# Kernel optimization log

Measured on AMD Instinct MI355X. Metric: run time of the kernel, lower is better.

The kernel has to match this reference:

```python
import jax, jax.numpy as jnp
import numpy as np

N_NODES = 50000
N_EDGES = 800000
H = 128            # node_hidden_size
T = 2              # num_prop_rounds


def setup_inputs() -> dict:
    key = jax.random.key(0)
    ks = jax.random.split(key, 10)
    hv = jax.random.normal(ks[0], (N_NODES, H), dtype=jnp.float32)
    he = jax.random.normal(ks[1], (N_EDGES, 1), dtype=jnp.float32)
    src = jax.random.randint(ks[2], (N_EDGES,), 0, N_NODES, dtype=jnp.int32)
    dst = jax.random.randint(ks[3], (N_EDGES,), 0, N_NODES, dtype=jnp.int32)
    # per-round params, stacked on leading T axis; small scale to avoid gate saturation
    W_msg = jax.random.normal(ks[4], (T, 2 * H, 2 * H + 1), dtype=jnp.float32) * 0.05
    b_msg = jax.random.normal(ks[5], (T, 2 * H), dtype=jnp.float32) * 0.05
    W_ih = jax.random.normal(ks[6], (T, 3 * H, 2 * H), dtype=jnp.float32) * 0.05
    W_hh = jax.random.normal(ks[7], (T, 3 * H, H), dtype=jnp.float32) * 0.05
    b_ih = jax.random.normal(ks[8], (T, 3 * H), dtype=jnp.float32) * 0.05
    b_hh = jax.random.normal(ks[9], (T, 3 * H), dtype=jnp.float32) * 0.05
    return dict(hv=hv, he=he, src=src, dst=dst, W_msg=W_msg, b_msg=b_msg,
                W_ih=W_ih, W_hh=W_hh, b_ih=b_ih, b_hh=b_hh)


def _gru_cell(x, h, W_ih, W_hh, b_ih, b_hh):
    # torch.nn.GRUCell math
    gi = x @ W_ih.T + b_ih          # [N, 3H]
    gh = h @ W_hh.T + b_hh          # [N, 3H]
    i_r, i_z, i_n = jnp.split(gi, 3, axis=1)
    h_r, h_z, h_n = jnp.split(gh, 3, axis=1)
    r = jax.nn.sigmoid(i_r + h_r)
    z = jax.nn.sigmoid(i_z + h_z)
    n = jnp.tanh(i_n + r * h_n)
    return (1.0 - z) * n + z * h


def reference(hv, he, src, dst, W_msg, b_msg, W_ih, W_hh, b_ih, b_hh):
    n_nodes = hv.shape[0]
    for t in range(T):
        # per-edge message input: concat([hv_dst, hv_src, he])  [E, 2H+1]
        msg_in = jnp.concatenate([hv[dst], hv[src], he], axis=1)
        edge_act = msg_in @ W_msg[t].T + b_msg[t]          # [E, 2H]
        # ragged sum-reduce over incoming edges (deg-0 nodes get zeros)
        a = jax.ops.segment_sum(edge_act, dst, num_segments=n_nodes)  # [N, 2H]
        hv = _gru_cell(a, hv, W_ih[t], W_hh[t], b_ih[t], b_hh[t])
    return hv
```

## Files before the change

### kernel.cpp

```cpp
#include <hip/hip_runtime.h>
#include <cstdint>
#include <cstddef>

#define N_NODES 50000
#define N_EDGES 800000
#define HDIM 128
#define TROUNDS 2
#define NTILES 3125
#define PACK_PER_T (416 * 64)
#define PACK_BLOCKS ((TROUNDS * PACK_PER_T) / 256)
#define CAST_BLOCKS ((N_NODES * HDIM / 4 + 255) / 256)
#define MAXDEG 64
#define NBUK 196
#define BCAP 4608
#define BCE 2048
#define NBC ((N_EDGES + BCE - 1) / BCE)

typedef __attribute__((ext_vector_type(8))) _Float16 half8v;
typedef __attribute__((ext_vector_type(2))) _Float16 half2v;
typedef __attribute__((ext_vector_type(4))) float f32x4;
typedef unsigned short ushort_t;
typedef unsigned long long u64;

#define GLD_LDS(gp, lp)                                                        \
  __builtin_amdgcn_global_load_lds(                                            \
      (__attribute__((address_space(1))) const void*)(gp),                     \
      (__attribute__((address_space(3))) void*)(lp), 16, 0, 0)

static __device__ __forceinline__ float sigmoidf_(float x) {
  return 1.0f / (1.0f + __expf(-x));
}
static __device__ __forceinline__ float tanhf_(float x) {
  float xc = fminf(15.0f, fmaxf(-15.0f, x));
  float a = __expf(2.0f * xc);
  return (a - 1.0f) / (a + 1.0f);
}
static __device__ __forceinline__ float f16bits2f(uint32_t hb) {
  ushort_t u = (ushort_t)hb;
  _Float16 h;
  __builtin_memcpy(&h, &u, 2);
  return (float)h;
}

__global__ void pack_cast(const float* __restrict__ Wmsg, const float* __restrict__ Wih,
                          const float* __restrict__ Whh, const float* __restrict__ hv,
                          _Float16* __restrict__ W1p, _Float16* __restrict__ W2p,
                          float* __restrict__ we, _Float16* __restrict__ hvh,
                          int* __restrict__ bcur) {
  if (blockIdx.x == 0 && threadIdx.x < NBUK) bcur[threadIdx.x] = 0;
  if (blockIdx.x >= PACK_BLOCKS) {
    int i = (blockIdx.x - PACK_BLOCKS) * 256 + threadIdx.x;
    if (i >= N_NODES * HDIM / 4) return;
    float4 v = reinterpret_cast<const float4*>(hv)[i];
    half2v o0, o1;
    o0[0] = (_Float16)v.x; o0[1] = (_Float16)v.y;
    o1[0] = (_Float16)v.z; o1[1] = (_Float16)v.w;
    reinterpret_cast<half2v*>(hvh)[i * 2] = o0;
    reinterpret_cast<half2v*>(hvh)[i * 2 + 1] = o1;
    return;
  }
  int g = blockIdx.x * 256 + threadIdx.x;
  if (g < TROUNDS * 256) {
    int t = g >> 8, j = g & 255;
    we[g] = Wmsg[((size_t)t * 256 + j) * 257 + 256];
  }
  int t = g / PACK_PER_T;
  int r = g % PACK_PER_T;
  int lane = r & 63;
  int fr = r >> 6;
  const float* srcp;
  _Float16* dstp;
  if (fr < 128) {
    int jt = fr >> 3, kt = fr & 7;
    int j = jt * 16 + (lane & 15);
    int k = kt * 32 + ((lane >> 4) << 3);
    srcp = Wmsg + (size_t)t * 256 * 257 + (size_t)j * 257 + k;
    dstp = W1p + ((size_t)t * 128 + fr) * 512 + lane * 8;
  } else {
    int fr2 = fr - 128;
    int chunk = fr2 / 12, idx = fr2 % 12;
    int jt = chunk / 3, pp = chunk % 3;
    int j = pp * 128 + jt * 16 + (lane & 15);
    int k;
    if (idx < 8) {
      k = idx * 32 + ((lane >> 4) << 3);
      srcp = Wih + (size_t)t * 384 * 256 + (size_t)j * 256 + k;
    } else {
      k = (idx - 8) * 32 + ((lane >> 4) << 3);
      srcp = Whh + (size_t)t * 384 * 128 + (size_t)j * 128 + k;
    }
    dstp = W2p + ((size_t)t * 288 + fr2) * 512 + lane * 8;
  }
  #pragma unroll
  for (int e = 0; e < 8; ++e) dstp[e] = (_Float16)srcp[e];
}

__global__ __launch_bounds__(256) void bin_count(
    const int* __restrict__ src, const int* __restrict__ dst,
    const float* __restrict__ he, int* __restrict__ bcur, u64* __restrict__ barr) {
  __shared__ int hist[256];
  __shared__ int incl[256];
  __shared__ int cur[256];
  __shared__ int gbase[256];
  __shared__ u64 staged[BCE];
  const int tid = threadIdx.x;
  const int e0 = blockIdx.x * BCE;
  const int tot = min(BCE, N_EDGES - e0);

  hist[tid] = 0;
  __syncthreads();

  u64 rec[BCE / 256];
  int nmine = 0;
  #pragma unroll
  for (int q = 0; q < BCE / 256; ++q) {
    int e = e0 + q * 256 + tid;
    if (e < N_EDGES) {
      uint32_t d = (uint32_t)dst[e];
      uint32_t s = (uint32_t)src[e];
      _Float16 hh = (_Float16)he[e];
      ushort_t hb;
      __builtin_memcpy(&hb, &hh, 2);
      rec[nmine] = ((u64)d << 32) | ((u64)hb << 16) | (u64)s;
      atomicAdd(&hist[d >> 8], 1);
      ++nmine;
    }
  }
  __syncthreads();

  incl[tid] = hist[tid];
  __syncthreads();
  for (int off = 1; off < 256; off <<= 1) {
    int v = incl[tid];
    int a = (tid >= off) ? incl[tid - off] : 0;
    __syncthreads();
    incl[tid] = v + a;
    __syncthreads();
  }
  cur[tid] = incl[tid] - hist[tid];
  __syncthreads();

  for (int q = 0; q < nmine; ++q) {
    int b = (int)(rec[q] >> 40);
    int pos = atomicAdd(&cur[b], 1);
    staged[pos] = rec[q];
  }
  if (tid < NBUK && hist[tid] > 0) gbase[tid] = atomicAdd(&bcur[tid], hist[tid]);
  __syncthreads();

  for (int i = tid; i < tot; i += 256) {
    u64 r = staged[i];
    int b = (int)(r >> 40);
    int excl = incl[b] - hist[b];
    barr[(size_t)b * BCAP + gbase[b] + (i - excl)] = r;
  }
}

__global__ __launch_bounds__(256) void bin_place(
    const int* __restrict__ bcur, const u64* __restrict__ barr,
    uint32_t* __restrict__ csr, int* __restrict__ deg_i) {
  __shared__ int lcnt[256];
  const int b = blockIdx.x;
  const int tid = threadIdx.x;
  const int cnt = bcur[b];
  lcnt[tid] = 0;
  __syncthreads();
  const u64* bp = barr + (size_t)b * BCAP;
  for (int i = tid; i < cnt; i += 256) {
    u64 r = bp[i];
    int d = (int)((r >> 32) & 0xffffu);
    int slot = atomicAdd(&lcnt[d & 255], 1);
    if (slot < MAXDEG) csr[(size_t)d * MAXDEG + slot] = (uint32_t)r;
  }
  __syncthreads();
  int node = b * 256 + tid;
  if (node < N_NODES) deg_i[node] = min(lcnt[tid], MAXDEG);
}

__global__ void gather_h(const _Float16* __restrict__ hvh, const int* __restrict__ deg_i,
                         const uint32_t* __restrict__ csr, _Float16* __restrict__ S_h,
                         float* __restrict__ hsum, float* __restrict__ deg_f, int n) {
  int wid = (int)((blockIdx.x * blockDim.x + threadIdx.x) >> 6);
  int lane = threadIdx.x & 63;
  if (wid >= n) return;
  int deg = deg_i[wid];
  uint32_t ent = (lane < deg) ? csr[(size_t)wid * MAXDEG + lane] : 0u;
  float a0 = 0.f, a1 = 0.f, hs = 0.f;
  int k = 0;
  for (; k + 7 < deg; k += 8) {
    uint32_t ee[8];
    #pragma unroll
    for (int q = 0; q < 8; ++q) ee[q] = __shfl(ent, k + q);
    half2v vv[8];
    #pragma unroll
    for (int q = 0; q < 8; ++q)
      vv[q] = *reinterpret_cast<const half2v*>(hvh + (size_t)(ee[q] & 0xffffu) * HDIM + lane * 2);
    #pragma unroll
    for (int q = 0; q < 8; ++q) {
      a0 += (float)vv[q][0];
      a1 += (float)vv[q][1];
      hs += f16bits2f(ee[q] >> 16);
    }
  }
  for (; k < deg; ++k) {
    uint32_t e0 = __shfl(ent, k);
    half2v v0 = *reinterpret_cast<const half2v*>(hvh + (size_t)(e0 & 0xffffu) * HDIM + lane * 2);
    a0 += (float)v0[0];
    a1 += (float)v0[1];
    hs += f16bits2f(e0 >> 16);
  }
  half2v o;
  o[0] = (_Float16)a0;
  o[1] = (_Float16)a1;
  *reinterpret_cast<half2v*>(S_h + (size_t)wid * HDIM + lane * 2) = o;
  if (lane == 0) hsum[wid] = hs;
  if (lane == 1) deg_f[wid] = (float)deg;
}

__global__ __launch_bounds__(256, 4) void u1_kernel(
    const _Float16* __restrict__ hvh, const _Float16* __restrict__ S_h,
    const float* __restrict__ deg_f, const float* __restrict__ hsum,
    const _Float16* __restrict__ W1p, const float* __restrict__ we,
    const float* __restrict__ bmsg, _Float16* __restrict__ a_out) {
  __shared__ _Float16 buf[2][16 * 512];
  const int tid = threadIdx.x;
  const int wv = tid >> 6, lane = tid & 63;
  const int tile = blockIdx.x * 4 + wv;
  const bool act = (tile < NTILES);
  const int rowA = tile * 16 + (lane & 15);
  const int koff = (lane >> 4) * 8;
  const int m0 = (lane >> 4) * 4;

  auto stage = [&](int ph) {
    const _Float16* g = W1p + (size_t)ph * 8192 + (size_t)(wv * 4) * 512 + lane * 8;
    _Float16* l = &buf[ph & 1][(wv * 4) * 512];
    #pragma unroll
    for (int i = 0; i < 4; ++i) GLD_LDS(g + i * 512, l + i * 512);
  };
  stage(0);

  half8v x[8];
  float degs[4], hss[4];
  if (act) {
    float deg = deg_f[rowA];
    const _Float16* hrow = hvh + (size_t)rowA * HDIM + koff;
    #pragma unroll
    for (int kt = 0; kt < 4; ++kt) {
      half8v hvv = *reinterpret_cast<const half8v*>(hrow + kt * 32);
      #pragma unroll
      for (int e = 0; e < 8; ++e) x[kt][e] = (_Float16)((float)hvv[e] * deg);
    }
    const _Float16* srow = S_h + (size_t)rowA * HDIM + koff;
    #pragma unroll
    for (int kt = 0; kt < 4; ++kt)
      x[4 + kt] = *reinterpret_cast<const half8v*>(srow + kt * 32);
    #pragma unroll
    for (int rr = 0; rr < 4; ++rr) {
      degs[rr] = deg_f[tile * 16 + m0 + rr];
      hss[rr] = hsum[tile * 16 + m0 + rr];
    }
  }

  #pragma unroll 1
  for (int ph = 0; ph < 8; ++ph) {
    __syncthreads();
    if (ph < 7) stage(ph + 1);
    #pragma unroll
    for (int half = 0; half < 2; ++half) {
      const _Float16* B = &buf[ph & 1][(size_t)half * 8 * 512];
      f32x4 acc = {0.f, 0.f, 0.f, 0.f};
      #pragma unroll
      for (int kt = 0; kt < 8; ++kt) {
        half8v b = *reinterpret_cast<const half8v*>(B + (size_t)kt * 512 + lane * 8);
        acc = __builtin_amdgcn_mfma_f32_16x16x32_f16(x[kt], b, acc, 0, 0, 0);
      }
      if (act) {
        int jt = ph * 2 + half;
        int j = jt * 16 + (lane & 15);
        float bm = bmsg[j], w = we[j];
        #pragma unroll
        for (int rr = 0; rr < 4; ++rr)
          a_out[(size_t)(tile * 16 + m0 + rr) * 256 + j] =
              (_Float16)(acc[rr] + degs[rr] * bm + hss[rr] * w);
      }
    }
  }
}

__global__ __launch_bounds__(256, 3) void u2_kernel(
    const _Float16* __restrict__ a_in, const _Float16* __restrict__ hvh_in,
    const _Float16* __restrict__ W2p, const float* __restrict__ bih,
    const float* __restrict__ bhh, float* __restrict__ hv_out,
    _Float16* __restrict__ hvh_out) {
  __shared__ _Float16 buf[2][24 * 512];
  const int tid = threadIdx.x;
  const int wv = tid >> 6, lane = tid & 63;
  const int tile = blockIdx.x * 4 + wv;
  const bool act = (tile < NTILES);
  const int rowA = tile * 16 + (lane & 15);
  const int koff = (lane >> 4) * 8;
  const int m0 = (lane >> 4) * 4;

  auto stage = [&](int ph) {
    const _Float16* g = W2p + (size_t)ph * 12288 + (size_t)(wv * 6) * 512 + lane * 8;
    _Float16* l = &buf[ph & 1][(wv * 6) * 512];
    #pragma unroll
    for (int i = 0; i < 6; ++i) GLD_LDS(g + i * 512, l + i * 512);
  };
  stage(0);

  half8v a8[8], h4[4];
  if (act) {
    const _Float16* ar = a_in + (size_t)rowA * 256 + koff;
    #pragma unroll
    for (int kt = 0; kt < 8; ++kt)
      a8[kt] = *reinterpret_cast<const half8v*>(ar + kt * 32);
    const _Float16* hr = hvh_in + (size_t)rowA * HDIM + koff;
    #pragma unroll
    for (int kt = 0; kt < 4; ++kt)
      h4[kt] = *reinterpret_cast<const half8v*>(hr + kt * 32);
  }

  auto compute = [&](const _Float16* B, f32x4& ai, f32x4& ag) {
    ai = (f32x4){0.f, 0.f, 0.f, 0.f};
    ag = (f32x4){0.f, 0.f, 0.f, 0.f};
    #pragma unroll
    for (int kt = 0; kt < 8; ++kt) {
      half8v b = *reinterpret_cast<const half8v*>(B + (size_t)kt * 512 + lane * 8);
      ai = __builtin_amdgcn_mfma_f32_16x16x32_f16(a8[kt], b, ai, 0, 0, 0);
    }
    #pragma unroll
    for (int kt = 0; kt < 4; ++kt) {
      half8v b = *reinterpret_cast<const half8v*>(B + (size_t)(8 + kt) * 512 + lane * 8);
      ag = __builtin_amdgcn_mfma_f32_16x16x32_f16(h4[kt], b, ag, 0, 0, 0);
    }
  };

  f32x4 rreg, zreg, ai, ag;
  #pragma unroll 1
  for (int ph = 0; ph < 12; ++ph) {
    __syncthreads();
    if (ph < 11) stage(ph + 1);
    #pragma unroll
    for (int half = 0; half < 2; ++half) {
      const int c = ph * 2 + half;
      const int jt = c / 3, p = c % 3;
      const int fcol = jt * 16 + (lane & 15);
      compute(&buf[ph & 1][(size_t)half * 12 * 512], ai, ag);
      if (act) {
        if (p == 0) {
          float bi = bih[fcol], bq = bhh[fcol];
          #pragma unroll
          for (int rr = 0; rr < 4; ++rr) rreg[rr] = sigmoidf_(ai[rr] + bi + ag[rr] + bq);
        } else if (p == 1) {
          float bi = bih[128 + fcol], bq = bhh[128 + fcol];
          #pragma unroll
          for (int rr = 0; rr < 4; ++rr) zreg[rr] = sigmoidf_(ai[rr] + bi + ag[rr] + bq);
        } else {
          float bi = bih[256 + fcol], bq = bhh[256 + fcol];
          #pragma unroll
          for (int rr = 0; rr < 4; ++rr) {
            int node = tile * 16 + m0 + rr;
            float n = tanhf_(ai[rr] + bi + rreg[rr] * (ag[rr] + bq));
            float h = (float)hvh_in[(size_t)node * HDIM + fcol];
            float hn = (1.f - zreg[rr]) * n + zreg[rr] * h;
            if (hv_out) hv_out[(size_t)node * HDIM + fcol] = hn;
            if (hvh_out) hvh_out[(size_t)node * HDIM + fcol] = (_Float16)hn;
          }
        }
      }
    }
  }
}

extern "C" void kernel_launch(void* const* d_in, const int* in_sizes, int n_in,
                              void* d_out, int out_size, void* d_ws, size_t ws_size,
                              hipStream_t stream) {
  const float* hv   = (const float*)d_in[0];
  const float* he   = (const float*)d_in[1];
  const int*   src  = (const int*)d_in[2];
  const int*   dst  = (const int*)d_in[3];
  const float* Wmsg = (const float*)d_in[4];
  const float* bmsg = (const float*)d_in[5];
  const float* Wih  = (const float*)d_in[6];
  const float* Whh  = (const float*)d_in[7];
  const float* bih  = (const float*)d_in[8];
  const float* bhh  = (const float*)d_in[9];

  char* p = (char*)d_ws;
  auto alloc = [&](size_t bytes) { char* r = p; p += (bytes + 255) & ~(size_t)255; return r; };
  _Float16* S_h   = (_Float16*)alloc((size_t)N_NODES * HDIM * 2);
  _Float16* a_buf = (_Float16*)alloc((size_t)N_NODES * 256 * 2);
  _Float16* hvh   = (_Float16*)alloc((size_t)N_NODES * HDIM * 2);
  float*    deg_f = (float*)alloc((size_t)N_NODES * 4);
  float*    hsum  = (float*)alloc((size_t)N_NODES * 4);
  float*    we    = (float*)alloc((size_t)TROUNDS * 256 * 4);
  const size_t W1PT = (size_t)128 * 512;
  const size_t W2PT = (size_t)288 * 512;
  _Float16* W1p = (_Float16*)alloc(TROUNDS * W1PT * 2);
  _Float16* W2p = (_Float16*)alloc(TROUNDS * W2PT * 2);
  int*      deg_i = (int*)alloc((size_t)N_NODES * 4);
  int*      bcur  = (int*)alloc((size_t)NBUK * 4);
  u64*      barr  = (u64*)alloc((size_t)NBUK * BCAP * 8);
  uint32_t* csr   = (uint32_t*)alloc((size_t)N_NODES * MAXDEG * 4);

  pack_cast<<<PACK_BLOCKS + CAST_BLOCKS, 256, 0, stream>>>(
      Wmsg, Wih, Whh, hv, W1p, W2p, we, hvh, bcur);
  bin_count<<<NBC, 256, 0, stream>>>(src, dst, he, bcur, barr);
  bin_place<<<NBUK, 256, 0, stream>>>(bcur, barr, csr, deg_i);

  float* outp = (float*)d_out;
  const int ugrid = (NTILES + 3) / 4;
  for (int t = 0; t < TROUNDS; ++t) {
    gather_h<<<(N_NODES + 3) / 4, 256, 0, stream>>>(hvh, deg_i, csr, S_h, hsum, deg_f, N_NODES);
    u1_kernel<<<ugrid, 256, 0, stream>>>(
        hvh, S_h, deg_f, hsum, W1p + (size_t)t * W1PT,
        we + (size_t)t * 256, bmsg + (size_t)t * 256, a_buf);
    u2_kernel<<<ugrid, 256, 0, stream>>>(
        a_buf, hvh, W2p + (size_t)t * W2PT,
        bih + (size_t)t * 384, bhh + (size_t)t * 384,
        (t == TROUNDS - 1) ? outp : (float*)nullptr,
        (t < TROUNDS - 1) ? hvh : (_Float16*)nullptr);
  }
  (void)in_sizes; (void)n_in; (void)out_size; (void)ws_size;
}
```

Baseline: 234.9 us.

## Triple-buffer GRU weight staging with vmcnt waits and defer output stores

The GRU update kernel now stages weights in 12-slab chunks into a 3-deep LDS ring, two chunks ahead, replacing the 2-deep 24-slab double buffer. A manual s_waitcnt vmcnt(3) plus raw barrier replaces __syncthreads so later prefetches can stay in flight. The n and z gate values are kept in registers, and all hidden-state loads and stores are moved to a final epilogue, so global loads no longer sit inside the pipeline. This raises register pressure with 64 extra floats per lane, which could lower occupancy below the declared 3 blocks per SM, and the vmcnt count assumes a particular ordering of memory operations.

```diff
diff --git a/kernel.cpp b/kernel.cpp
--- a/kernel.cpp
+++ b/kernel.cpp
@@ -292,7 +292,7 @@
     const _Float16* __restrict__ W2p, const float* __restrict__ bih,
     const float* __restrict__ bhh, float* __restrict__ hv_out,
     _Float16* __restrict__ hvh_out) {
-  __shared__ _Float16 buf[2][24 * 512];
+  __shared__ _Float16 buf[3][12 * 512];
   const int tid = threadIdx.x;
   const int wv = tid >> 6, lane = tid & 63;
   const int tile = blockIdx.x * 4 + wv;
@@ -301,14 +301,6 @@
   const int koff = (lane >> 4) * 8;
   const int m0 = (lane >> 4) * 4;
 
-  auto stage = [&](int ph) {
-    const _Float16* g = W2p + (size_t)ph * 12288 + (size_t)(wv * 6) * 512 + lane * 8;
-    _Float16* l = &buf[ph & 1][(wv * 6) * 512];
-    #pragma unroll
-    for (int i = 0; i < 6; ++i) GLD_LDS(g + i * 512, l + i * 512);
-  };
-  stage(0);
-
   half8v a8[8], h4[4];
   if (act) {
     const _Float16* ar = a_in + (size_t)rowA * 256 + koff;
@@ -321,6 +313,15 @@
       h4[kt] = *reinterpret_cast<const half8v*>(hr + kt * 32);
   }
 
+  auto stage = [&](int c) {
+    const _Float16* g = W2p + (size_t)c * 6144 + (size_t)(wv * 3) * 512 + lane * 8;
+    _Float16* l = &buf[c % 3][(wv * 3) * 512];
+    #pragma unroll
+    for (int i = 0; i < 3; ++i) GLD_LDS(g + i * 512, l + i * 512);
+  };
+  stage(0);
+  stage(1);
+
   auto compute = [&](const _Float16* B, f32x4& ai, f32x4& ag) {
     ai = (f32x4){0.f, 0.f, 0.f, 0.f};
     ag = (f32x4){0.f, 0.f, 0.f, 0.f};
@@ -336,17 +337,19 @@
     }
   };
 
-  f32x4 rreg, zreg, ai, ag;
-  #pragma unroll 1
-  for (int ph = 0; ph < 12; ++ph) {
-    __syncthreads();
-    if (ph < 11) stage(ph + 1);
-    #pragma unroll
-    for (int half = 0; half < 2; ++half) {
-      const int c = ph * 2 + half;
-      const int jt = c / 3, p = c % 3;
-      const int fcol = jt * 16 + (lane & 15);
-      compute(&buf[ph & 1][(size_t)half * 12 * 512], ai, ag);
+  f32x4 rreg, ai, ag;
+  f32x4 nsave[8], zsave[8];
+  #pragma unroll
+  for (int jt = 0; jt < 8; ++jt) {
+    const int fcol = jt * 16 + (lane & 15);
+    #pragma unroll
+    for (int p = 0; p < 3; ++p) {
+      const int c = jt * 3 + p;
+      asm volatile("s_waitcnt vmcnt(3)" ::: "memory");
+      __builtin_amdgcn_s_barrier();
+      __builtin_amdgcn_sched_barrier(0);
+      if (c < 22) stage(c + 2);
+      compute(&buf[c % 3][0], ai, ag);
       if (act) {
         if (p == 0) {
           float bi = bih[fcol], bq = bhh[fcol];
@@ -355,19 +358,28 @@
         } else if (p == 1) {
           float bi = bih[128 + fcol], bq = bhh[128 + fcol];
           #pragma unroll
-          for (int rr = 0; rr < 4; ++rr) zreg[rr] = sigmoidf_(ai[rr] + bi + ag[rr] + bq);
+          for (int rr = 0; rr < 4; ++rr) zsave[jt][rr] = sigmoidf_(ai[rr] + bi + ag[rr] + bq);
         } else {
           float bi = bih[256 + fcol], bq = bhh[256 + fcol];
           #pragma unroll
-          for (int rr = 0; rr < 4; ++rr) {
-            int node = tile * 16 + m0 + rr;
-            float n = tanhf_(ai[rr] + bi + rreg[rr] * (ag[rr] + bq));
-            float h = (float)hvh_in[(size_t)node * HDIM + fcol];
-            float hn = (1.f - zreg[rr]) * n + zreg[rr] * h;
-            if (hv_out) hv_out[(size_t)node * HDIM + fcol] = hn;
-            if (hvh_out) hvh_out[(size_t)node * HDIM + fcol] = (_Float16)hn;
-          }
+          for (int rr = 0; rr < 4; ++rr)
+            nsave[jt][rr] = tanhf_(ai[rr] + bi + rreg[rr] * (ag[rr] + bq));
         }
+      }
+    }
+  }
+
+  if (act) {
+    #pragma unroll
+    for (int jt = 0; jt < 8; ++jt) {
+      const int fcol = jt * 16 + (lane & 15);
+      #pragma unroll
+      for (int rr = 0; rr < 4; ++rr) {
+        int node = tile * 16 + m0 + rr;
+        float h = (float)hvh_in[(size_t)node * HDIM + fcol];
+        float hn = (1.f - zsave[jt][rr]) * nsave[jt][rr] + zsave[jt][rr] * h;
+        if (hv_out) hv_out[(size_t)node * HDIM + fcol] = hn;
+        if (hvh_out) hvh_out[(size_t)node * HDIM + fcol] = (_Float16)hn;
       }
     }
   }
```

Result: no change. 232.8 us (-0.9%).
